# Optimization experiments

Measured on AMD Instinct MI355X. Metric: run time of the kernel, lower is better.

## Reference

```python
import jax, jax.numpy as jnp
import numpy as np

N, D, T, P, NP, H = 200000, 128, 8, 2000, 9, 2048


def setup_inputs() -> dict:
    key = jax.random.key(0)
    ks = jax.random.split(key, 12)
    inp = {
        'motion_z': jax.random.normal(ks[0], (N, D), jnp.float32),
        'tasks': jax.random.randint(ks[1], (N,), 0, T, jnp.int32),
        'tasks_mask': jax.random.randint(ks[2], (N,), 0, 2, jnp.int32),
        'patient_ids': jax.random.randint(ks[3], (N,), 0, P, jnp.int32),
        'phenos': jax.random.uniform(ks[4], (N, NP), jnp.float32),
        'phenos_mask': jax.random.randint(ks[5], (N,), 0, 2, jnp.int32),
        'W1': jax.random.normal(ks[6], (T * D, H), jnp.float32) * 0.02,
        'b1': jnp.zeros((H,), jnp.float32),
        'W2': jax.random.normal(ks[7], (H, H), jnp.float32) * 0.02,
        'b2': jnp.zeros((H,), jnp.float32),
        'W3': jax.random.normal(ks[8], (H, NP), jnp.float32) * 0.02,
        'b3': jnp.zeros((NP,), jnp.float32),
    }
    return inp


def _fingerprint(motion_z, tasks, tasks_mask, patient_ids, phenos, phenos_mask):
    # valid sample mask (tasks_mask==1 & patient id present & phenos_mask==1)
    valid = (tasks_mask == 1) & (phenos_mask == 1)
    w = valid.astype(motion_z.dtype)                      # [N]
    wz = motion_z * w[:, None]                            # [N, D]

    # global per-task mean (fallback for empty patient-task cells)
    t_sum = jax.ops.segment_sum(wz, tasks, num_segments=T)           # [T, D]
    t_cnt = jax.ops.segment_sum(w, tasks, num_segments=T)            # [T]
    task_mean = t_sum / jnp.maximum(t_cnt, 1.0)[:, None]             # [T, D]

    # fused (patient, task) segment mean — single pass scatter-reduce
    seg = patient_ids * T + tasks                                    # [N]
    pt_sum = jax.ops.segment_sum(wz, seg, num_segments=P * T)        # [P*T, D]
    pt_cnt = jax.ops.segment_sum(w, seg, num_segments=P * T)         # [P*T]
    pt_mean = pt_sum / jnp.maximum(pt_cnt, 1.0)[:, None]
    pt_mean = jnp.where((pt_cnt > 0)[:, None], pt_mean,
                        jnp.tile(task_mean, (P, 1)))                 # fallback
    fingerprint = pt_mean.reshape(P, T * D)

    # first valid pheno row per patient (phenos_id_each[0])
    idxs = jnp.where(valid, jnp.arange(N), N)
    first = jnp.full((P,), N, jnp.int32).at[patient_ids].min(idxs.astype(jnp.int32))
    uni_phenos = phenos[jnp.clip(first, 0, N - 1)]                   # [P, NP]
    return fingerprint, uni_phenos


def reference(motion_z, tasks, tasks_mask, patient_ids, phenos, phenos_mask,
              W1, b1, W2, b2, W3, b3):
    fingerprint, uni_phenos = _fingerprint(
        motion_z, tasks, tasks_mask, patient_ids, phenos, phenos_mask)
    h = jax.nn.relu(fingerprint @ W1 + b1)
    h = jax.nn.relu(h @ W2 + b2)
    pheno_latent = h @ W3 + b3
    out = jax.nn.sigmoid(pheno_latent)
    return out, uni_phenos, pheno_latent
```

## Files before the change

### kernel.cpp

```cpp
#include <hip/hip_runtime.h>
#include <math.h>

#define N_SAMP 200000
#define D_     128
#define T_     8
#define P_     2000
#define NP_    9
#define H_     2048
#define MPAD   2048
#define NSEG   16000

#define OFF_PTSUM   0
#define OFF_CNT     8192000
#define OFF_TSUM    8256000
#define OFF_TCNT    8260096
#define OFF_FMAX    8260352
#define ZERO_BYTES  8268352
#define OFF_FPHI    8268544
#define OFF_FPLO    12462848
#define OFF_W1THI   16657152
#define OFF_W1TLO   20851456
#define OFF_H1HI    25045760
#define OFF_H1LO    33434368
#define OFF_W2THI   41822976
#define OFF_W2TLO   50211584
#define OFF_H2      OFF_FPHI

typedef __attribute__((ext_vector_type(8))) short bf16x8;
typedef __attribute__((ext_vector_type(4))) float f32x4;

__device__ __forceinline__ unsigned f2bf_rne(float x) {
    unsigned b = __float_as_uint(x);
    return (b + 0x7fffu + ((b >> 16) & 1u)) >> 16;
}
__device__ __forceinline__ float bf2f(unsigned u) {
    return __uint_as_float(u << 16);
}

__device__ __forceinline__ void gload16(const void* g, void* l) {
    __builtin_amdgcn_global_load_lds(
        (const __attribute__((address_space(1))) unsigned int*)g,
        (__attribute__((address_space(3))) unsigned int*)l, 16, 0, 0);
}

__global__ __launch_bounds__(256) void scatter_pt(
    const float* __restrict__ motion_z, const int* __restrict__ tasks,
    const int* __restrict__ tmask, const int* __restrict__ pids,
    const int* __restrict__ pmask, float* __restrict__ pt_sum,
    float* __restrict__ cnt, unsigned* __restrict__ fmax)
{
    int wid0 = (blockIdx.x * blockDim.x + threadIdx.x) >> 6;
    int lane = threadIdx.x & 63;
    int nw   = (gridDim.x * blockDim.x) >> 6;
    for (int wid = wid0; wid < N_SAMP; wid += nw) {
        if (tmask[wid] != 1 || pmask[wid] != 1) continue;
        int p = pids[wid];
        int seg = p * T_ + tasks[wid];
        if (lane == 0) {
            atomicAdd(&cnt[seg], 1.0f);
            atomicMax(&fmax[p], (unsigned)(N_SAMP - wid));
        }
        float2 v = *(const float2*)&motion_z[(size_t)wid * D_ + lane * 2];
        atomicAdd(&pt_sum[seg * D_ + lane * 2 + 0], v.x);
        atomicAdd(&pt_sum[seg * D_ + lane * 2 + 1], v.y);
    }
}

__global__ __launch_bounds__(256) void tsum_partial(
    const float* __restrict__ pt_sum, const float* __restrict__ cnt,
    float* __restrict__ tsum, float* __restrict__ tcnt)
{
    int p0 = blockIdx.x * 16;
    int tid = threadIdx.x;
    float4 acc = make_float4(0.f, 0.f, 0.f, 0.f);
    for (int pl = 0; pl < 16; ++pl) {
        float4 v = *(const float4*)&pt_sum[(size_t)(p0 + pl) * 1024 + tid * 4];
        acc.x += v.x; acc.y += v.y; acc.z += v.z; acc.w += v.w;
    }
    atomicAdd(&tsum[tid * 4 + 0], acc.x);
    atomicAdd(&tsum[tid * 4 + 1], acc.y);
    atomicAdd(&tsum[tid * 4 + 2], acc.z);
    atomicAdd(&tsum[tid * 4 + 3], acc.w);
    if (tid < 128) {
        int p = p0 + (tid >> 3), t = tid & 7;
        atomicAdd(&tcnt[t], cnt[p * 8 + t]);
    }
}

__global__ __launch_bounds__(256) void finalize_fused(
    const float* __restrict__ pt_sum, const float* __restrict__ cnt,
    const float* __restrict__ tsum, const float* __restrict__ tcnt,
    const unsigned* __restrict__ fmax, const float* __restrict__ phenos,
    unsigned short* __restrict__ fphi, unsigned short* __restrict__ fplo,
    float* __restrict__ uni)
{
    int e = blockIdx.x * 256 + threadIdx.x;
    if (e < MPAD * 1024) {
        int p = e >> 10, col = e & 1023;
        float v = 0.f;
        if (p < P_) {
            float c = cnt[p * T_ + (col >> 7)];
            v = (c > 0.f) ? pt_sum[e] / c
                          : tsum[col] / fmaxf(tcnt[col >> 7], 1.0f);
        }
        unsigned hi = f2bf_rne(v);
        fphi[e] = (unsigned short)hi;
        fplo[e] = (unsigned short)f2bf_rne(v - bf2f(hi));
    } else {
        int g = e - MPAD * 1024;
        if (g < P_ * NP_) {
            int p = g / NP_, j = g - p * NP_;
            unsigned fm = fmax[p];
            int idx = fm ? (int)(N_SAMP - fm) : N_SAMP - 1;
            uni[g] = phenos[(size_t)idx * NP_ + j];
        }
    }
}

__global__ __launch_bounds__(256) void conv_w_both(
    const float* __restrict__ W1, const float* __restrict__ W2,
    unsigned short* __restrict__ w1hi, unsigned short* __restrict__ w1lo,
    unsigned short* __restrict__ w2hi, unsigned short* __restrict__ w2lo)
{
    __shared__ float tile[32][33];
    int id = blockIdx.x;
    const float* W; unsigned short *Whi, *Wlo; int K;
    if (id < 2048) { W = W1; Whi = w1hi; Wlo = w1lo; K = 1024; }
    else { id -= 2048; W = W2; Whi = w2hi; Wlo = w2lo; K = 2048; }
    int bx = id & 63, by = id >> 6;
    int k0 = by * 32, n0 = bx * 32;
    const int N = 2048;
    int r = threadIdx.x >> 3, c4 = (threadIdx.x & 7) * 4;
    float4 v = *(const float4*)&W[(size_t)(k0 + r) * N + n0 + c4];
    tile[r][c4 + 0] = v.x; tile[r][c4 + 1] = v.y;
    tile[r][c4 + 2] = v.z; tile[r][c4 + 3] = v.w;
    __syncthreads();
    unsigned short hi[4], lo[4];
#pragma unroll
    for (int q = 0; q < 4; ++q) {
        float x = tile[c4 + q][r];
        unsigned h = f2bf_rne(x);
        hi[q] = (unsigned short)h;
        lo[q] = (unsigned short)f2bf_rne(x - bf2f(h));
    }
    size_t o = (size_t)(n0 + r) * K + k0 + c4;
    *(ushort4*)&Whi[o] = make_ushort4(hi[0], hi[1], hi[2], hi[3]);
    *(ushort4*)&Wlo[o] = make_ushort4(lo[0], lo[1], lo[2], lo[3]);
}

template<int OUTF32>
__global__ __launch_bounds__(256, 1) void gemm_split(
    const unsigned short* __restrict__ Ahi, const unsigned short* __restrict__ Alo,
    const unsigned short* __restrict__ Bhi, const unsigned short* __restrict__ Blo,
    const float* __restrict__ bias,
    float* __restrict__ Cf, unsigned short* __restrict__ Chi,
    unsigned short* __restrict__ Clo, int K)
{
    __shared__ __align__(16) char lds[2][4][8192];
    int tid  = threadIdx.x;
    int lane = tid & 63, w = tid >> 6;
    int wr = w >> 1, wc = w & 1;
    int row0 = blockIdx.y * 128, col0 = blockIdx.x * 128;

    int fr = lane & 15;
    int fk = (lane >> 4) * 8;

    const unsigned short* srcs[4] = {Ahi, Alo, Bhi, Blo};
    int base0[4] = {row0, row0, col0, col0};

    auto STAGE = [&](int buf, int t) {
        int k0 = t * 32;
#pragma unroll
        for (int pc = 0; pc < 4; ++pc) {
#pragma unroll
            for (int rep = 0; rep < 2; ++rep) {
                int tile = rep * 4 + w;
                const unsigned short* g =
                    srcs[pc] + (size_t)(base0[pc] + tile * 16 + fr) * K + k0 + fk;
                gload16(g, &lds[buf][pc][tile * 1024]);
            }
        }
    };

    f32x4 acc[4][4] = {};
    int nt = K / 32;
    STAGE(0, 0);
    __syncthreads();
    int cur = 0;
    int lo16 = lane * 16;

    for (int t = 0; t < nt; ++t) {
        if (t + 1 < nt) STAGE(cur ^ 1, t + 1);
        bf16x8 ah[4], al[4], bh[4], bl[4];
#pragma unroll
        for (int i = 0; i < 4; ++i) {
            ah[i] = *(const bf16x8*)&lds[cur][0][(wr * 4 + i) * 1024 + lo16];
            al[i] = *(const bf16x8*)&lds[cur][1][(wr * 4 + i) * 1024 + lo16];
        }
#pragma unroll
        for (int j = 0; j < 4; ++j) {
            bh[j] = *(const bf16x8*)&lds[cur][2][(wc * 4 + j) * 1024 + lo16];
            bl[j] = *(const bf16x8*)&lds[cur][3][(wc * 4 + j) * 1024 + lo16];
        }
#pragma unroll
        for (int i = 0; i < 4; ++i)
#pragma unroll
            for (int j = 0; j < 4; ++j) {
                acc[i][j] = __builtin_amdgcn_mfma_f32_16x16x32_bf16(ah[i], bh[j], acc[i][j], 0, 0, 0);
                acc[i][j] = __builtin_amdgcn_mfma_f32_16x16x32_bf16(ah[i], bl[j], acc[i][j], 0, 0, 0);
                acc[i][j] = __builtin_amdgcn_mfma_f32_16x16x32_bf16(al[i], bh[j], acc[i][j], 0, 0, 0);
            }
        __syncthreads();
        cur ^= 1;
    }

#pragma unroll
    for (int i = 0; i < 4; ++i) {
        int r = row0 + wr * 64 + i * 16 + (lane >> 4) * 4;
#pragma unroll
        for (int j = 0; j < 4; ++j) {
            int c = col0 + wc * 64 + j * 16 + (lane & 15);
            float bv = bias[c];
#pragma unroll
            for (int q = 0; q < 4; ++q) {
                float x = fmaxf(acc[i][j][q] + bv, 0.f);
                size_t o = (size_t)(r + q) * H_ + c;
                if (OUTF32) {
                    Cf[o] = x;
                } else {
                    unsigned hb = f2bf_rne(x);
                    Chi[o] = (unsigned short)hb;
                    Clo[o] = (unsigned short)f2bf_rne(x - bf2f(hb));
                }
            }
        }
    }
}

__global__ __launch_bounds__(256) void out_head(
    const float* __restrict__ h2, const float* __restrict__ W3,
    const float* __restrict__ b3, float* __restrict__ out,
    float* __restrict__ latent)
{
    __shared__ float w3s[H_ * NP_];
    int tid = threadIdx.x;
    for (int e = tid * 4; e < H_ * NP_; e += 1024)
        *(float4*)&w3s[e] = *(const float4*)&W3[e];
    __syncthreads();

    int wid  = blockIdx.x * 4 + (tid >> 6);
    int lane = tid & 63;
    if (wid >= P_) return;
    const float* hrow = h2 + (size_t)wid * H_;
    float acc[NP_] = {};
    for (int k = lane; k < H_; k += 64) {
        float h = hrow[k];
#pragma unroll
        for (int j = 0; j < NP_; ++j) acc[j] = fmaf(h, w3s[k * NP_ + j], acc[j]);
    }
#pragma unroll
    for (int off = 32; off > 0; off >>= 1)
#pragma unroll
        for (int j = 0; j < NP_; ++j) acc[j] += __shfl_down(acc[j], off);
    if (lane == 0) {
#pragma unroll
        for (int j = 0; j < NP_; ++j) {
            float v = acc[j] + b3[j];
            latent[wid * NP_ + j] = v;
            out[wid * NP_ + j]    = 1.f / (1.f + expf(-v));
        }
    }
}

extern "C" void kernel_launch(void* const* d_in, const int* in_sizes, int n_in,
                              void* d_out, int out_size, void* d_ws, size_t ws_size,
                              hipStream_t stream)
{
    const float* motion_z = (const float*)d_in[0];
    const int*   tasks    = (const int*)d_in[1];
    const int*   tmask    = (const int*)d_in[2];
    const int*   pids     = (const int*)d_in[3];
    const float* phenos   = (const float*)d_in[4];
    const int*   pmask    = (const int*)d_in[5];
    const float* W1 = (const float*)d_in[6];
    const float* b1 = (const float*)d_in[7];
    const float* W2 = (const float*)d_in[8];
    const float* b2 = (const float*)d_in[9];
    const float* W3 = (const float*)d_in[10];
    const float* b3 = (const float*)d_in[11];

    char* ws = (char*)d_ws;
    float*          pt_sum = (float*)(ws + OFF_PTSUM);
    float*          cnt    = (float*)(ws + OFF_CNT);
    float*          tsum   = (float*)(ws + OFF_TSUM);
    float*          tcnt   = (float*)(ws + OFF_TCNT);
    unsigned*       fmax   = (unsigned*)(ws + OFF_FMAX);
    unsigned short* fphi   = (unsigned short*)(ws + OFF_FPHI);
    unsigned short* fplo   = (unsigned short*)(ws + OFF_FPLO);
    unsigned short* w1thi  = (unsigned short*)(ws + OFF_W1THI);
    unsigned short* w1tlo  = (unsigned short*)(ws + OFF_W1TLO);
    unsigned short* h1hi   = (unsigned short*)(ws + OFF_H1HI);
    unsigned short* h1lo   = (unsigned short*)(ws + OFF_H1LO);
    unsigned short* w2thi  = (unsigned short*)(ws + OFF_W2THI);
    unsigned short* w2tlo  = (unsigned short*)(ws + OFF_W2TLO);
    float*          h2     = (float*)(ws + OFF_H2);

    float* out    = (float*)d_out;
    float* uni    = out + P_ * NP_;
    float* latent = out + 2 * P_ * NP_;

    hipMemsetAsync(ws, 0, ZERO_BYTES, stream);

    scatter_pt<<<2048, 256, 0, stream>>>(motion_z, tasks, tmask, pids, pmask,
                                         pt_sum, cnt, fmax);
    tsum_partial<<<125, 256, 0, stream>>>(pt_sum, cnt, tsum, tcnt);
    finalize_fused<<<(MPAD * 1024 + P_ * NP_ + 255) / 256, 256, 0, stream>>>(
        pt_sum, cnt, tsum, tcnt, fmax, phenos, fphi, fplo, uni);

    conv_w_both<<<6144, 256, 0, stream>>>(W1, W2, w1thi, w1tlo, w2thi, w2tlo);

    gemm_split<0><<<dim3(16, 16), 256, 0, stream>>>(
        fphi, fplo, w1thi, w1tlo, b1, nullptr, h1hi, h1lo, 1024);
    gemm_split<1><<<dim3(16, 16), 256, 0, stream>>>(
        h1hi, h1lo, w2thi, w2tlo, b2, h2, nullptr, nullptr, H_);

    out_head<<<P_ / 4, 256, 0, stream>>>(h2, W3, b3, out, latent);
}
```

Before: 438.2 us.

## Compact valid samples in scatter, fuse tsum with weight conversion, vectorize finalize

The scatter kernel now reads the masks for a whole 256-sample chunk in parallel and compacts the valid samples into a shared list. Waves then process only the valid rows, instead of one wave per sample doing serial mask loads. The task-sum reduction and the W1/W2 bf16 split-transpose are merged into one launch so they share a kernel and overlap, which removes one launch. Finalize now handles 8 elements per thread with float4 loads and ushort4 stores. The cost is extra block-level syncs in the scatter and a more heterogeneous fused kernel.

```diff
diff --git a/kernel.cpp b/kernel.cpp
--- a/kernel.cpp
+++ b/kernel.cpp
@@ -49,42 +49,86 @@
     const int* __restrict__ pmask, float* __restrict__ pt_sum,
     float* __restrict__ cnt, unsigned* __restrict__ fmax)
 {
-    int wid0 = (blockIdx.x * blockDim.x + threadIdx.x) >> 6;
-    int lane = threadIdx.x & 63;
-    int nw   = (gridDim.x * blockDim.x) >> 6;
-    for (int wid = wid0; wid < N_SAMP; wid += nw) {
-        if (tmask[wid] != 1 || pmask[wid] != 1) continue;
-        int p = pids[wid];
-        int seg = p * T_ + tasks[wid];
-        if (lane == 0) {
+    __shared__ unsigned list[256];
+    __shared__ int nvalid;
+    int tid  = threadIdx.x;
+    int lane = tid & 63;
+    int wv   = tid >> 6;
+    for (int base = blockIdx.x * 256; base < N_SAMP; base += gridDim.x * 256) {
+        if (tid == 0) nvalid = 0;
+        __syncthreads();
+        int i = base + tid;
+        if (i < N_SAMP && tmask[i] == 1 && pmask[i] == 1) {
+            int p = pids[i];
+            int seg = p * T_ + tasks[i];
             atomicAdd(&cnt[seg], 1.0f);
-            atomicMax(&fmax[p], (unsigned)(N_SAMP - wid));
-        }
-        float2 v = *(const float2*)&motion_z[(size_t)wid * D_ + lane * 2];
-        atomicAdd(&pt_sum[seg * D_ + lane * 2 + 0], v.x);
-        atomicAdd(&pt_sum[seg * D_ + lane * 2 + 1], v.y);
-    }
-}
-
-__global__ __launch_bounds__(256) void tsum_partial(
+            atomicMax(&fmax[p], (unsigned)(N_SAMP - i));
+            int pos = atomicAdd(&nvalid, 1);
+            list[pos] = ((unsigned)seg << 18) | (unsigned)i;
+        }
+        __syncthreads();
+        int nv = nvalid;
+        for (int e = wv; e < nv; e += 4) {
+            unsigned pk = list[e];
+            int row = (int)(pk & 0x3FFFFu);
+            int seg = (int)(pk >> 18);
+            float2 v = *(const float2*)&motion_z[(size_t)row * D_ + lane * 2];
+            atomicAdd(&pt_sum[seg * D_ + lane * 2 + 0], v.x);
+            atomicAdd(&pt_sum[seg * D_ + lane * 2 + 1], v.y);
+        }
+        __syncthreads();
+    }
+}
+
+__global__ __launch_bounds__(256) void mid_fused(
     const float* __restrict__ pt_sum, const float* __restrict__ cnt,
-    float* __restrict__ tsum, float* __restrict__ tcnt)
-{
-    int p0 = blockIdx.x * 16;
+    float* __restrict__ tsum, float* __restrict__ tcnt,
+    const float* __restrict__ W1, const float* __restrict__ W2,
+    unsigned short* __restrict__ w1hi, unsigned short* __restrict__ w1lo,
+    unsigned short* __restrict__ w2hi, unsigned short* __restrict__ w2lo)
+{
+    __shared__ float tile[32][33];
     int tid = threadIdx.x;
-    float4 acc = make_float4(0.f, 0.f, 0.f, 0.f);
-    for (int pl = 0; pl < 16; ++pl) {
-        float4 v = *(const float4*)&pt_sum[(size_t)(p0 + pl) * 1024 + tid * 4];
-        acc.x += v.x; acc.y += v.y; acc.z += v.z; acc.w += v.w;
-    }
-    atomicAdd(&tsum[tid * 4 + 0], acc.x);
-    atomicAdd(&tsum[tid * 4 + 1], acc.y);
-    atomicAdd(&tsum[tid * 4 + 2], acc.z);
-    atomicAdd(&tsum[tid * 4 + 3], acc.w);
-    if (tid < 128) {
-        int p = p0 + (tid >> 3), t = tid & 7;
-        atomicAdd(&tcnt[t], cnt[p * 8 + t]);
-    }
+    if (blockIdx.x < 125) {
+        int p0 = blockIdx.x * 16;
+        float4 acc = make_float4(0.f, 0.f, 0.f, 0.f);
+        for (int pl = 0; pl < 16; ++pl) {
+            float4 v = *(const float4*)&pt_sum[(size_t)(p0 + pl) * 1024 + tid * 4];
+            acc.x += v.x; acc.y += v.y; acc.z += v.z; acc.w += v.w;
+        }
+        atomicAdd(&tsum[tid * 4 + 0], acc.x);
+        atomicAdd(&tsum[tid * 4 + 1], acc.y);
+        atomicAdd(&tsum[tid * 4 + 2], acc.z);
+        atomicAdd(&tsum[tid * 4 + 3], acc.w);
+        if (tid < 128) {
+            int p = p0 + (tid >> 3), t = tid & 7;
+            atomicAdd(&tcnt[t], cnt[p * 8 + t]);
+        }
+        return;
+    }
+    int id = blockIdx.x - 125;
+    const float* W; unsigned short *Whi, *Wlo; int K;
+    if (id < 2048) { W = W1; Whi = w1hi; Wlo = w1lo; K = 1024; }
+    else { id -= 2048; W = W2; Whi = w2hi; Wlo = w2lo; K = 2048; }
+    int bx = id & 63, by = id >> 6;
+    int k0 = by * 32, n0 = bx * 32;
+    const int N = 2048;
+    int r = tid >> 3, c4 = (tid & 7) * 4;
+    float4 v = *(const float4*)&W[(size_t)(k0 + r) * N + n0 + c4];
+    tile[r][c4 + 0] = v.x; tile[r][c4 + 1] = v.y;
+    tile[r][c4 + 2] = v.z; tile[r][c4 + 3] = v.w;
+    __syncthreads();
+    unsigned short hi[4], lo[4];
+#pragma unroll
+    for (int q = 0; q < 4; ++q) {
+        float x = tile[c4 + q][r];
+        unsigned h = f2bf_rne(x);
+        hi[q] = (unsigned short)h;
+        lo[q] = (unsigned short)f2bf_rne(x - bf2f(h));
+    }
+    size_t o = (size_t)(n0 + r) * K + k0 + c4;
+    *(ushort4*)&Whi[o] = make_ushort4(hi[0], hi[1], hi[2], hi[3]);
+    *(ushort4*)&Wlo[o] = make_ushort4(lo[0], lo[1], lo[2], lo[3]);
 }
 
 __global__ __launch_bounds__(256) void finalize_fused(
@@ -94,20 +138,36 @@
     unsigned short* __restrict__ fphi, unsigned short* __restrict__ fplo,
     float* __restrict__ uni)
 {
-    int e = blockIdx.x * 256 + threadIdx.x;
-    if (e < MPAD * 1024) {
-        int p = e >> 10, col = e & 1023;
-        float v = 0.f;
+    if (blockIdx.x < 1024) {
+        int e8 = blockIdx.x * 256 + threadIdx.x;
+        int e  = e8 * 8;
+        int p = e >> 10, col0 = e & 1023;
+        int seg = p * T_ + (col0 >> 7);
+        ushort hi[8], lo[8];
         if (p < P_) {
-            float c = cnt[p * T_ + (col >> 7)];
-            v = (c > 0.f) ? pt_sum[e] / c
-                          : tsum[col] / fmaxf(tcnt[col >> 7], 1.0f);
-        }
-        unsigned hi = f2bf_rne(v);
-        fphi[e] = (unsigned short)hi;
-        fplo[e] = (unsigned short)f2bf_rne(v - bf2f(hi));
+            float c = cnt[seg];
+            float4 a = *(const float4*)&pt_sum[e];
+            float4 b = *(const float4*)&pt_sum[e + 4];
+            float vv[8] = {a.x, a.y, a.z, a.w, b.x, b.y, b.z, b.w};
+#pragma unroll
+            for (int q = 0; q < 8; ++q) {
+                float v;
+                if (c > 0.f) v = vv[q] / c;
+                else         v = tsum[col0 + q] / fmaxf(tcnt[col0 >> 7], 1.0f);
+                unsigned h = f2bf_rne(v);
+                hi[q] = (ushort)h;
+                lo[q] = (ushort)f2bf_rne(v - bf2f(h));
+            }
+        } else {
+#pragma unroll
+            for (int q = 0; q < 8; ++q) { hi[q] = 0; lo[q] = 0; }
+        }
+        *(ushort4*)&fphi[e]     = make_ushort4(hi[0], hi[1], hi[2], hi[3]);
+        *(ushort4*)&fphi[e + 4] = make_ushort4(hi[4], hi[5], hi[6], hi[7]);
+        *(ushort4*)&fplo[e]     = make_ushort4(lo[0], lo[1], lo[2], lo[3]);
+        *(ushort4*)&fplo[e + 4] = make_ushort4(lo[4], lo[5], lo[6], lo[7]);
     } else {
-        int g = e - MPAD * 1024;
+        int g = (blockIdx.x - 1024) * 256 + threadIdx.x;
         if (g < P_ * NP_) {
             int p = g / NP_, j = g - p * NP_;
             unsigned fm = fmax[p];
@@ -115,37 +175,6 @@
             uni[g] = phenos[(size_t)idx * NP_ + j];
         }
     }
-}
-
-__global__ __launch_bounds__(256) void conv_w_both(
-    const float* __restrict__ W1, const float* __restrict__ W2,
-    unsigned short* __restrict__ w1hi, unsigned short* __restrict__ w1lo,
-    unsigned short* __restrict__ w2hi, unsigned short* __restrict__ w2lo)
-{
-    __shared__ float tile[32][33];
-    int id = blockIdx.x;
-    const float* W; unsigned short *Whi, *Wlo; int K;
-    if (id < 2048) { W = W1; Whi = w1hi; Wlo = w1lo; K = 1024; }
-    else { id -= 2048; W = W2; Whi = w2hi; Wlo = w2lo; K = 2048; }
-    int bx = id & 63, by = id >> 6;
-    int k0 = by * 32, n0 = bx * 32;
-    const int N = 2048;
-    int r = threadIdx.x >> 3, c4 = (threadIdx.x & 7) * 4;
-    float4 v = *(const float4*)&W[(size_t)(k0 + r) * N + n0 + c4];
-    tile[r][c4 + 0] = v.x; tile[r][c4 + 1] = v.y;
-    tile[r][c4 + 2] = v.z; tile[r][c4 + 3] = v.w;
-    __syncthreads();
-    unsigned short hi[4], lo[4];
-#pragma unroll
-    for (int q = 0; q < 4; ++q) {
-        float x = tile[c4 + q][r];
-        unsigned h = f2bf_rne(x);
-        hi[q] = (unsigned short)h;
-        lo[q] = (unsigned short)f2bf_rne(x - bf2f(h));
-    }
-    size_t o = (size_t)(n0 + r) * K + k0 + c4;
-    *(ushort4*)&Whi[o] = make_ushort4(hi[0], hi[1], hi[2], hi[3]);
-    *(ushort4*)&Wlo[o] = make_ushort4(lo[0], lo[1], lo[2], lo[3]);
 }
 
 template<int OUTF32>
@@ -311,13 +340,12 @@
 
     hipMemsetAsync(ws, 0, ZERO_BYTES, stream);
 
-    scatter_pt<<<2048, 256, 0, stream>>>(motion_z, tasks, tmask, pids, pmask,
-                                         pt_sum, cnt, fmax);
-    tsum_partial<<<125, 256, 0, stream>>>(pt_sum, cnt, tsum, tcnt);
-    finalize_fused<<<(MPAD * 1024 + P_ * NP_ + 255) / 256, 256, 0, stream>>>(
+    scatter_pt<<<782, 256, 0, stream>>>(motion_z, tasks, tmask, pids, pmask,
+                                        pt_sum, cnt, fmax);
+    mid_fused<<<125 + 6144, 256, 0, stream>>>(pt_sum, cnt, tsum, tcnt,
+                                              W1, W2, w1thi, w1tlo, w2thi, w2tlo);
+    finalize_fused<<<1024 + (P_ * NP_ + 255) / 256, 256, 0, stream>>>(
         pt_sum, cnt, tsum, tcnt, fmax, phenos, fphi, fplo, uni);
-
-    conv_w_both<<<6144, 256, 0, stream>>>(W1, W2, w1thi, w1tlo, w2thi, w2tlo);
 
     gemm_split<0><<<dim3(16, 16), 256, 0, stream>>>(
         fphi, fplo, w1thi, w1tlo, b1, nullptr, h1hi, h1lo, 1024);
```

Result: faster. 420.8 us (-4.0%).
